# Optimization experiments

Hardware: AMD Instinct MI355X
Metric: run time of the kernel (lower is better)

## Reference

```python
import jax, jax.numpy as jnp
import numpy as np

D_MODEL = 2048
D_FF = 4096
N_EXPERTS = 8
TOP_K = 2
ALPHA = 0.01


def setup_inputs() -> dict:
    key = jax.random.key(0)
    ks = jax.random.split(key, 5)
    x = jax.random.normal(ks[0], (1, 2048, D_MODEL), dtype=jnp.float32)
    Wr = jax.random.normal(ks[1], (N_EXPERTS, D_MODEL), dtype=jnp.float32) * 0.01
    W1 = jax.random.normal(ks[2], (N_EXPERTS, D_MODEL, D_FF), dtype=jnp.float32) * (D_MODEL ** -0.5)
    W3 = jax.random.normal(ks[3], (N_EXPERTS, D_MODEL, D_FF), dtype=jnp.float32) * (D_MODEL ** -0.5)
    W2 = jax.random.normal(ks[4], (N_EXPERTS, D_FF, D_MODEL), dtype=jnp.float32) * (D_FF ** -0.5)
    return {"x": x, "Wr": Wr, "W1": W1, "W3": W3, "W2": W2}


def reference(x, Wr, W1, W3, W2):
    B, S, D = x.shape
    xf = x.reshape(-1, D)                      # [N, D]
    N = xf.shape[0]
    E = Wr.shape[0]
    logits = xf @ Wr.T                          # [N, E]
    probs = jax.nn.softmax(logits, axis=-1)
    tk_p, tk_i = jax.lax.top_k(probs, TOP_K)    # [N, K]
    tk_p = tk_p / tk_p.sum(axis=-1, keepdims=True)
    # combine weights per (token, expert); scatter-add matches masked sum over k
    w = jnp.zeros((N, E), x.dtype).at[jnp.arange(N)[:, None], tk_i].add(tk_p)
    # dense per-expert SwiGLU FFN (zero-weighted experts contribute nothing)
    gate = jnp.einsum('nd,edf->enf', xf, W1)    # [E, N, F]
    up = jnp.einsum('nd,edf->enf', xf, W3)
    expert_out = jnp.einsum('enf,efd->end', jax.nn.silu(gate) * up, W2)  # [E, N, D]
    out = jnp.einsum('ne,end->nd', w, expert_out).reshape(B, S, D)
    # load-balancing aux loss
    counts = jnp.zeros(E, x.dtype).at[tk_i.ravel()].add(1.0)
    f_i = counts / (N * TOP_K)
    P_i = probs.mean(axis=0)
    aux_loss = ALPHA * E * jnp.sum(f_i * P_i)
    return out, aux_loss
```

## Files before the change

kernel.cpp:

```cpp
#include <hip/hip_runtime.h>
#include <hip/hip_bf16.h>
#include <math.h>

#define D_MODEL 2048
#define D_FF    4096
#define NTOK    2048
#define NEXP    8
#define NPAIR   (NTOK*2)
#define MAXTILES 48

typedef __hip_bfloat16 bf16;
using frag_ab = __attribute__((ext_vector_type(8))) short;
using frag_cd = __attribute__((ext_vector_type(4))) float;

__device__ __forceinline__ short f2bf_s(float f) {
  __hip_bfloat16 h = __float2bfloat16(f);
  union { __hip_bfloat16 b; short s; } u; u.b = h; return u.s;
}
__device__ __forceinline__ short4 f2bf4(const float4 v) {
  short4 r; r.x = f2bf_s(v.x); r.y = f2bf_s(v.y); r.z = f2bf_s(v.z); r.w = f2bf_s(v.w);
  return r;
}
__device__ __forceinline__ frag_ab pack8(const float4 v0, const float4 v1) {
  frag_ab r;
  r[0] = f2bf_s(v0.x); r[1] = f2bf_s(v0.y); r[2] = f2bf_s(v0.z); r[3] = f2bf_s(v0.w);
  r[4] = f2bf_s(v1.x); r[5] = f2bf_s(v1.y); r[6] = f2bf_s(v1.z); r[7] = f2bf_s(v1.w);
  return r;
}
__device__ __forceinline__ void gload_lds16(const void* g, void* l) {
  __builtin_amdgcn_global_load_lds(
      (const __attribute__((address_space(1))) unsigned int*)g,
      (__attribute__((address_space(3))) unsigned int*)l, 16, 0, 0);
}

__global__ void k_zero(int* cnt, int* cur, float* psum) {
  int t = threadIdx.x;
  if (t < NEXP) { cnt[t] = 0; cur[t] = 0; psum[t] = 0.f; }
}

__global__ void k_route(const float* __restrict__ x, const float* __restrict__ Wr,
                        int* __restrict__ tki, float* __restrict__ tkw,
                        int* __restrict__ cnt, float* __restrict__ psum) {
  const int n = blockIdx.x;
  const int t = threadIdx.x;
  const float* xr = x + (size_t)n * D_MODEL;
  float acc[NEXP];
#pragma unroll
  for (int e = 0; e < NEXP; e++) acc[e] = 0.f;
  for (int d = t; d < D_MODEL; d += 256) {
    float xv = xr[d];
#pragma unroll
    for (int e = 0; e < NEXP; e++) acc[e] += xv * Wr[e * D_MODEL + d];
  }
  __shared__ float red[256 * NEXP];
#pragma unroll
  for (int e = 0; e < NEXP; e++) red[t * NEXP + e] = acc[e];
  __syncthreads();
  __shared__ float logit[NEXP];
  if (t < NEXP) {
    float s = 0.f;
    for (int i = 0; i < 256; i++) s += red[i * NEXP + t];
    logit[t] = s;
  }
  __syncthreads();
  if (t == 0) {
    float m = logit[0];
#pragma unroll
    for (int e = 1; e < NEXP; e++) m = fmaxf(m, logit[e]);
    float p[NEXP]; float s = 0.f;
#pragma unroll
    for (int e = 0; e < NEXP; e++) { p[e] = expf(logit[e] - m); s += p[e]; }
    float inv = 1.f / s;
#pragma unroll
    for (int e = 0; e < NEXP; e++) p[e] *= inv;
    int i0 = 0;
#pragma unroll
    for (int e = 1; e < NEXP; e++) if (p[e] > p[i0]) i0 = e;
    int i1 = (i0 == 0) ? 1 : 0;
#pragma unroll
    for (int e = 0; e < NEXP; e++) if (e != i0 && e != i1 && p[e] > p[i1]) i1 = e;
    float wsum = p[i0] + p[i1];
    tki[n*2]   = i0;          tki[n*2+1] = i1;
    tkw[n*2]   = p[i0]/wsum;  tkw[n*2+1] = p[i1]/wsum;
    atomicAdd(&cnt[i0], 1);   atomicAdd(&cnt[i1], 1);
#pragma unroll
    for (int e = 0; e < NEXP; e++) atomicAdd(&psum[e], p[e]);
  }
}

__global__ void k_scan(const int* __restrict__ cnt, const float* __restrict__ psum,
                       int* __restrict__ off, int* __restrict__ te, int* __restrict__ tm,
                       float* __restrict__ aux_out) {
  if (threadIdx.x != 0) return;
  int o = 0;
  for (int e = 0; e < NEXP; e++) { off[e] = o; o += cnt[e]; }
  off[NEXP] = o;
  int nt = 0;
  for (int e = 0; e < NEXP; e++)
    for (int msv = 0; msv < cnt[e]; msv += 128) { te[nt] = e; tm[nt] = msv; nt++; }
  for (; nt < MAXTILES; nt++) { te[nt] = -1; tm[nt] = 0; }
  float aux = 0.f;
  for (int e = 0; e < NEXP; e++)
    aux += ((float)cnt[e] / (float)NPAIR) * (psum[e] / (float)NTOK);
  aux_out[0] = aux * 0.01f * (float)NEXP;
}

__global__ void k_assign(const int* __restrict__ tki, const float* __restrict__ tkw,
                         const int* __restrict__ off, int* __restrict__ cur,
                         int* __restrict__ perm, float* __restrict__ pw,
                         int* __restrict__ posof) {
  int n = blockIdx.x * blockDim.x + threadIdx.x;
  if (n >= NTOK) return;
#pragma unroll
  for (int k = 0; k < 2; k++) {
    int e = tki[n*2+k];
    int r = atomicAdd(&cur[e], 1);
    int pos = off[e] + r;
    perm[pos] = n;
    pw[pos]   = tkw[n*2+k];
    posof[n*2+k] = pos;
  }
}

template<int K, int F>
__device__ __forceinline__ void tpose_body(const float* __restrict__ s,
                                           char* __restrict__ d,
                                           int k0, int f0, int t, float* T ) {
#pragma unroll
  for (int i = 0; i < 8; i++) {
    int sl = t + i * 256;
    int kr = sl >> 4, q4 = sl & 15;
    float4 v = *(const float4*)(s + (size_t)(k0 + kr) * F + f0 + q4 * 4);
    int qs = q4 ^ ((kr >> 3) & 7);
    *(float4*)(&T[kr * 64 + qs * 4]) = v;
  }
  __syncthreads();
#pragma unroll
  for (int i = 0; i < 4; i++) {
    int sl = t + i * 256;
    int fr = sl >> 4, cg = sl & 15;
    int g = cg >> 3, c = cg & 7;
    int l = c ^ (fr & 7);
    int rbase = g * 64 + l * 8;
    int col = (fr & 3) + (((fr >> 2) ^ l) << 2);
    frag_ab r;
#pragma unroll
    for (int j = 0; j < 8; j++) r[j] = f2bf_s(T[(rbase + j) * 64 + col]);
    *(frag_ab*)(d + (size_t)(f0 + fr) * K * 2 + (size_t)k0 * 2 + g * 128 + c * 16) = r;
  }
}

template<int K, int F>
__global__ __launch_bounds__(256) void k_tpose(const float* __restrict__ src,
                                               bf16* __restrict__ dst) {
  __shared__ __align__(16) float T[128 * 64];
  const int e = blockIdx.z;
  tpose_body<K, F>(src + (size_t)e * K * F, (char*)(dst + (size_t)e * F * K),
                   blockIdx.y * 128, blockIdx.x * 64, threadIdx.x, T);
}

template<int K, int F>
__global__ __launch_bounds__(256) void k_tpose_dual(const float* __restrict__ srcA,
                                                    const float* __restrict__ srcB,
                                                    bf16* __restrict__ dstA,
                                                    bf16* __restrict__ dstB) {
  __shared__ __align__(16) float T[128 * 64];
  const int e = blockIdx.z & 7;
  const float* src = (blockIdx.z & 8) ? srcB : srcA;
  bf16*        dst = (blockIdx.z & 8) ? dstB : dstA;
  tpose_body<K, F>(src + (size_t)e * K * F, (char*)(dst + (size_t)e * F * K),
                   blockIdx.y * 128, blockIdx.x * 64, threadIdx.x, T);
}

__global__ __launch_bounds__(256, 2) void k_gemm1n(
    const float* __restrict__ x, const bf16* __restrict__ W1b,
    const bf16* __restrict__ W3b,
    const int* __restrict__ perm, const int* __restrict__ off,
    const int* __restrict__ tile_e, const int* __restrict__ tile_m,
    const int* __restrict__ cnt, bf16* __restrict__ H) {
  const int e = tile_e[blockIdx.y];
  if (e < 0) return;
  const int ms = tile_m[blockIdx.y];
  int mrows = cnt[e] - ms; if (mrows > 128) mrows = 128;
  const int f0 = blockIdx.x * 128;
  const int base = off[e] + ms;

  __shared__ __align__(16) bf16 As [128 * 64];
  __shared__ __align__(16) bf16 B1s[128 * 64];
  __shared__ __align__(16) bf16 B3s[128 * 64];
  __shared__ int permS[128];

  const int t = threadIdx.x;
  const int lane = t & 63;
  const int wuni = t & 192;
  const int wid = t >> 6;
  const int wm = wid & 1, wn = wid >> 1;
  const int lm = lane & 15, q = lane >> 4;

  if (t < 128) permS[t] = (t < mrows) ? perm[base + t] : 0;

  frag_cd accg[4][4], accu[4][4];
#pragma unroll
  for (int i = 0; i < 4; i++)
#pragma unroll
    for (int j = 0; j < 4; j++) {
      accg[i][j] = {0.f,0.f,0.f,0.f};
      accu[i][j] = {0.f,0.f,0.f,0.f};
    }

  const char* W1e = (const char*)(W1b + (size_t)e * D_MODEL * D_FF);
  const char* W3e = (const char*)(W3b + (size_t)e * D_MODEL * D_FF);
  __syncthreads();

  for (int k0 = 0; k0 < D_MODEL; k0 += 64) {
#pragma unroll
    for (int i = 0; i < 4; i++) {
      int wslot = i * 256 + wuni;
      int slot  = wslot + lane;
      int row = slot >> 3, c = slot & 7;
      size_t gb = (size_t)(f0 + row) * (D_MODEL * 2) + (size_t)k0 * 2 + c * 16;
      gload_lds16(W1e + gb, &B1s[wslot * 8]);
      gload_lds16(W3e + gb, &B3s[wslot * 8]);
    }
#pragma unroll
    for (int i = 0; i < 4; i++) {
      int slot = i * 256 + t;
      int row = slot >> 3, c = slot & 7;
      int tok = permS[row];
      const float4* p = (const float4*)(x + (size_t)tok * D_MODEL + k0 + c * 8);
      frag_ab v = pack8(p[0], p[1]);
      *(frag_ab*)(&As[row * 64 + ((c ^ (row & 7)) * 8)]) = v;
    }
    __syncthreads();
#pragma unroll
    for (int ks = 0; ks < 2; ks++) {
      frag_ab a[4], b1[4], b3[4];
#pragma unroll
      for (int mf = 0; mf < 4; mf++) {
        int row = wm*64 + mf*16 + lm;
        int c = (ks*4 + q) ^ (row & 7);
        a[mf] = *(const frag_ab*)(&As[row * 64 + c * 8]);
      }
#pragma unroll
      for (int nf = 0; nf < 4; nf++) {
        int row = wn*64 + nf*16 + lm;
        int c = (ks*4 + q) ^ (row & 7);
        b1[nf] = *(const frag_ab*)(&B1s[row * 64 + c * 8]);
        b3[nf] = *(const frag_ab*)(&B3s[row * 64 + c * 8]);
      }
#pragma unroll
      for (int mf = 0; mf < 4; mf++)
#pragma unroll
        for (int nf = 0; nf < 4; nf++) {
          accg[mf][nf] = __builtin_amdgcn_mfma_f32_16x16x32_bf16(a[mf], b1[nf], accg[mf][nf], 0, 0, 0);
          accu[mf][nf] = __builtin_amdgcn_mfma_f32_16x16x32_bf16(a[mf], b3[nf], accu[mf][nf], 0, 0, 0);
        }
    }
    __syncthreads();
  }
#pragma unroll
  for (int mf = 0; mf < 4; mf++) {
#pragma unroll
    for (int r = 0; r < 4; r++) {
      int row = wm*64 + mf*16 + q*4 + r;
      if (row < mrows) {
        char* hrow = (char*)H + (size_t)(base + row) * (D_FF * 2);
        int key = row & 7;
#pragma unroll
        for (int nf = 0; nf < 4; nf++) {
          float g = accg[mf][nf][r];
          float u = accu[mf][nf][r];
          float h = g * u / (1.f + expf(-g));
          int f = f0 + wn*64 + nf*16 + lm;
          int grp = f >> 6, oct = (f >> 3) & 7, j = f & 7;
          *(bf16*)(hrow + grp*128 + ((oct ^ key) * 16) + j*2) = __float2bfloat16(h);
        }
      }
    }
  }
}

__global__ __launch_bounds__(256, 3) void k_gemm2n(
    const bf16* __restrict__ H, const bf16* __restrict__ W2b,
    const float* __restrict__ pw,
    const int* __restrict__ off, const int* __restrict__ tile_e,
    const int* __restrict__ tile_m, const int* __restrict__ cnt,
    float* __restrict__ eo) {
  const int e = tile_e[blockIdx.y];
  if (e < 0) return;
  const int ms = tile_m[blockIdx.y];
  int mrows = cnt[e] - ms; if (mrows > 128) mrows = 128;
  const int d0 = blockIdx.x * 128;
  const int base = off[e] + ms;

  __shared__ __align__(16) bf16 As[128 * 64];
  __shared__ __align__(16) bf16 Bs[128 * 64];

  const int t = threadIdx.x;
  const int lane = t & 63;
  const int wuni = t & 192;
  const int wid = t >> 6;
  const int wm = wid & 1, wn = wid >> 1;
  const int lm = lane & 15, q = lane >> 4;

  frag_cd acc[4][4];
#pragma unroll
  for (int i = 0; i < 4; i++)
#pragma unroll
    for (int j = 0; j < 4; j++) acc[i][j] = {0.f,0.f,0.f,0.f};

  const char* W2e = (const char*)(W2b + (size_t)e * D_FF * D_MODEL);
  const char* Hb  = (const char*)H;

  for (int k0 = 0; k0 < D_FF; k0 += 64) {
#pragma unroll
    for (int i = 0; i < 4; i++) {
      int wslot = i * 256 + wuni;
      int slot  = wslot + lane;
      int row = slot >> 3, c = slot & 7;
      gload_lds16(Hb + (size_t)(base + row) * (D_FF * 2) + (size_t)k0 * 2 + c * 16,
                  &As[wslot * 8]);
      gload_lds16(W2e + (size_t)(d0 + row) * (D_FF * 2) + (size_t)k0 * 2 + c * 16,
                  &Bs[wslot * 8]);
    }
    __syncthreads();
#pragma unroll
    for (int ks = 0; ks < 2; ks++) {
      frag_ab a[4], b[4];
#pragma unroll
      for (int mf = 0; mf < 4; mf++) {
        int row = wm*64 + mf*16 + lm;
        int c = (ks*4 + q) ^ (row & 7);
        a[mf] = *(const frag_ab*)(&As[row * 64 + c * 8]);
      }
#pragma unroll
      for (int nf = 0; nf < 4; nf++) {
        int row = wn*64 + nf*16 + lm;
        int c = (ks*4 + q) ^ (row & 7);
        b[nf] = *(const frag_ab*)(&Bs[row * 64 + c * 8]);
      }
#pragma unroll
      for (int mf = 0; mf < 4; mf++)
#pragma unroll
        for (int nf = 0; nf < 4; nf++)
          acc[mf][nf] = __builtin_amdgcn_mfma_f32_16x16x32_bf16(a[mf], b[nf], acc[mf][nf], 0, 0, 0);
    }
    __syncthreads();
  }
#pragma unroll
  for (int mf = 0; mf < 4; mf++) {
#pragma unroll
    for (int r = 0; r < 4; r++) {
      int row = wm*64 + mf*16 + q*4 + r;
      if (row < mrows) {
        float w = pw[base + row];
        float* orow = eo + (size_t)(base + row) * D_MODEL;
#pragma unroll
        for (int nf = 0; nf < 4; nf++)
          orow[d0 + wn*64 + nf*16 + lm] = w * acc[mf][nf][r];
      }
    }
  }
}

__global__ __launch_bounds__(256) void k_gemm1(
    const float* __restrict__ x, const float* __restrict__ W1,
    const float* __restrict__ W3,
    const int* __restrict__ perm, const int* __restrict__ off,
    const int* __restrict__ tile_e, const int* __restrict__ tile_m,
    const int* __restrict__ cnt, bf16* __restrict__ H) {
  const int e = tile_e[blockIdx.y];
  if (e < 0) return;
  const int ms = tile_m[blockIdx.y];
  int mrows = cnt[e] - ms; if (mrows > 128) mrows = 128;
  const int f0 = blockIdx.x * 128;
  const int base = off[e] + ms;

  __shared__ __align__(16) bf16 As [128 * 40];
  __shared__ __align__(16) bf16 B1s[128 * 40];
  __shared__ __align__(16) bf16 B3s[128 * 40];
  __shared__ int permS[128];

  const int t = threadIdx.x;
  const int lane = t & 63, wid = t >> 6;
  const int wm = wid & 1, wn = wid >> 1;
  const int lm = lane & 15, q = lane >> 4;

  if (t < 128) permS[t] = (t < mrows) ? perm[base + t] : 0;

  frag_cd accg[4][4], accu[4][4];
#pragma unroll
  for (int i = 0; i < 4; i++)
#pragma unroll
    for (int j = 0; j < 4; j++) {
      accg[i][j] = {0.f,0.f,0.f,0.f};
      accu[i][j] = {0.f,0.f,0.f,0.f};
    }

  const float* W1e = W1 + (size_t)e * D_MODEL * D_FF;
  const float* W3e = W3 + (size_t)e * D_MODEL * D_FF;
  __syncthreads();

  for (int k0 = 0; k0 < D_MODEL; k0 += 32) {
#pragma unroll
    for (int i = 0; i < 4; i++) {
      int s = t + i * 256;
      int row = s >> 3, kg = s & 7;
      float4 v = make_float4(0.f, 0.f, 0.f, 0.f);
      if (row < mrows) {
        int tok = permS[row];
        v = *(const float4*)(x + (size_t)tok * D_MODEL + k0 + kg * 4);
      }
      *(short4*)(&As[row * 40 + kg * 4]) = f2bf4(v);
    }
#pragma unroll
    for (int i = 0; i < 2; i++) {
      int s = t + i * 256;
      int f = s & 127, kg = s >> 7;
      const float* g1 = W1e + (size_t)(k0 + kg * 8) * D_FF + f0 + f;
      const float* g3 = W3e + (size_t)(k0 + kg * 8) * D_FF + f0 + f;
      short r1[8], r3[8];
#pragma unroll
      for (int j = 0; j < 8; j++) r1[j] = f2bf_s(g1[(size_t)j * D_FF]);
#pragma unroll
      for (int j = 0; j < 8; j++) r3[j] = f2bf_s(g3[(size_t)j * D_FF]);
      *(frag_ab*)(&B1s[f * 40 + kg * 8]) = *(const frag_ab*)r1;
      *(frag_ab*)(&B3s[f * 40 + kg * 8]) = *(const frag_ab*)r3;
    }
    __syncthreads();
    frag_ab a[4], b1[4], b3[4];
#pragma unroll
    for (int mf = 0; mf < 4; mf++)
      a[mf] = *(const frag_ab*)(&As[(wm*64 + mf*16 + lm) * 40 + q*8]);
#pragma unroll
    for (int nf = 0; nf < 4; nf++) {
      b1[nf] = *(const frag_ab*)(&B1s[(wn*64 + nf*16 + lm) * 40 + q*8]);
      b3[nf] = *(const frag_ab*)(&B3s[(wn*64 + nf*16 + lm) * 40 + q*8]);
    }
#pragma unroll
    for (int mf = 0; mf < 4; mf++)
#pragma unroll
      for (int nf = 0; nf < 4; nf++) {
        accg[mf][nf] = __builtin_amdgcn_mfma_f32_16x16x32_bf16(a[mf], b1[nf], accg[mf][nf], 0, 0, 0);
        accu[mf][nf] = __builtin_amdgcn_mfma_f32_16x16x32_bf16(a[mf], b3[nf], accu[mf][nf], 0, 0, 0);
      }
    __syncthreads();
  }
#pragma unroll
  for (int mf = 0; mf < 4; mf++) {
#pragma unroll
    for (int r = 0; r < 4; r++) {
      int row = wm*64 + mf*16 + q*4 + r;
      if (row < mrows) {
        bf16* hrow = H + (size_t)(base + row) * D_FF;
#pragma unroll
        for (int nf = 0; nf < 4; nf++) {
          float g = accg[mf][nf][r];
          float u = accu[mf][nf][r];
          float h = g * u / (1.f + expf(-g));
          hrow[f0 + wn*64 + nf*16 + lm] = __float2bfloat16(h);
        }
      }
    }
  }
}

__global__ __launch_bounds__(256) void k_gemm2(
    const bf16* __restrict__ H, const float* __restrict__ W2,
    const float* __restrict__ pw,
    const int* __restrict__ off, const int* __restrict__ tile_e,
    const int* __restrict__ tile_m, const int* __restrict__ cnt,
    float* __restrict__ eo) {
  const int e = tile_e[blockIdx.y];
  if (e < 0) return;
  const int ms = tile_m[blockIdx.y];
  int mrows = cnt[e] - ms; if (mrows > 128) mrows = 128;
  const int d0 = blockIdx.x * 128;
  const int base = off[e] + ms;

  __shared__ __align__(16) bf16 As[128 * 40];
  __shared__ __align__(16) bf16 Bs[128 * 40];

  const int t = threadIdx.x;
  const int lane = t & 63, wid = t >> 6;
  const int wm = wid & 1, wn = wid >> 1;
  const int lm = lane & 15, q = lane >> 4;

  frag_cd acc[4][4];
#pragma unroll
  for (int i = 0; i < 4; i++)
#pragma unroll
    for (int j = 0; j < 4; j++) acc[i][j] = {0.f,0.f,0.f,0.f};

  const float* W2e = W2 + (size_t)e * D_FF * D_MODEL;
  const short* Hs = (const short*)H;

  for (int k0 = 0; k0 < D_FF; k0 += 32) {
#pragma unroll
    for (int i = 0; i < 2; i++) {
      int s = t + i * 256;
      int row = s >> 2, kg = s & 3;
      frag_ab v = {0,0,0,0,0,0,0,0};
      if (row < mrows)
        v = *(const frag_ab*)(Hs + (size_t)(base + row) * D_FF + k0 + kg * 8);
      *(frag_ab*)(&As[row * 40 + kg * 8]) = v;
    }
#pragma unroll
    for (int i = 0; i < 2; i++) {
      int s = t + i * 256;
      int dd = s & 127, kg = s >> 7;
      const float* g2 = W2e + (size_t)(k0 + kg * 8) * D_MODEL + d0 + dd;
      short r2[8];
#pragma unroll
      for (int j = 0; j < 8; j++) r2[j] = f2bf_s(g2[(size_t)j * D_MODEL]);
      *(frag_ab*)(&Bs[dd * 40 + kg * 8]) = *(const frag_ab*)r2;
    }
    __syncthreads();
    frag_ab a[4], b[4];
#pragma unroll
    for (int mf = 0; mf < 4; mf++)
      a[mf] = *(const frag_ab*)(&As[(wm*64 + mf*16 + lm) * 40 + q*8]);
#pragma unroll
    for (int nf = 0; nf < 4; nf++)
      b[nf] = *(const frag_ab*)(&Bs[(wn*64 + nf*16 + lm) * 40 + q*8]);
#pragma unroll
    for (int mf = 0; mf < 4; mf++)
#pragma unroll
      for (int nf = 0; nf < 4; nf++)
        acc[mf][nf] = __builtin_amdgcn_mfma_f32_16x16x32_bf16(a[mf], b[nf], acc[mf][nf], 0, 0, 0);
    __syncthreads();
  }
#pragma unroll
  for (int mf = 0; mf < 4; mf++) {
#pragma unroll
    for (int r = 0; r < 4; r++) {
      int row = wm*64 + mf*16 + q*4 + r;
      if (row < mrows) {
        float w = pw[base + row];
        float* orow = eo + (size_t)(base + row) * D_MODEL;
#pragma unroll
        for (int nf = 0; nf < 4; nf++)
          orow[d0 + wn*64 + nf*16 + lm] = w * acc[mf][nf][r];
      }
    }
  }
}

__global__ void k_combine(const float* __restrict__ eo, const int* __restrict__ posof,
                          float* __restrict__ out) {
  int idx = blockIdx.x * 256 + threadIdx.x;
  int n = idx >> 9;
  int c = (idx & 511) * 4;
  int p0 = posof[n*2], p1 = posof[n*2+1];
  const float4 a = *(const float4*)(eo + (size_t)p0 * D_MODEL + c);
  const float4 b = *(const float4*)(eo + (size_t)p1 * D_MODEL + c);
  float4 r;
  r.x = a.x + b.x; r.y = a.y + b.y; r.z = a.z + b.z; r.w = a.w + b.w;
  *(float4*)(out + (size_t)n * D_MODEL + c) = r;
}

extern "C" void kernel_launch(void* const* d_in, const int* in_sizes, int n_in,
                              void* d_out, int out_size, void* d_ws, size_t ws_size,
                              hipStream_t stream) {
  const float* x  = (const float*)d_in[0];
  const float* Wr = (const float*)d_in[1];
  const float* W1 = (const float*)d_in[2];
  const float* W3 = (const float*)d_in[3];
  const float* W2 = (const float*)d_in[4];
  float* out = (float*)d_out;
  char* ws = (char*)d_ws;

  const size_t REQ = (290ull << 20);
  if (ws_size >= REQ) {
    bf16*  W1b = (bf16*)(ws);
    bf16*  W3b = (bf16*)(ws + (128ull << 20));
    bf16*  Hb  = (bf16*)(ws + (256ull << 20));
    bf16*  W2b = (bf16*)(ws);
    float* eo  = (float*)(ws + (128ull << 20));
    char*  ib  = ws + (289ull << 20);
    int*   perm  = (int*)(ib);
    float* pw    = (float*)(ib + 16384);
    int*   posof = (int*)(ib + 32768);
    int*   tki   = (int*)(ib + 49152);
    float* tkw   = (float*)(ib + 65536);
    int*   cnt   = (int*)(ib + 81920);
    int*   cur   = (int*)(ib + 82048);
    int*   off   = (int*)(ib + 82176);
    int*   te    = (int*)(ib + 82432);
    int*   tm    = (int*)(ib + 82688);
    float* psum  = (float*)(ib + 82944);

    k_zero<<<1, 64, 0, stream>>>(cnt, cur, psum);
    k_route<<<NTOK, 256, 0, stream>>>(x, Wr, tki, tkw, cnt, psum);
    k_scan<<<1, 1, 0, stream>>>(cnt, psum, off, te, tm, out + (size_t)NTOK * D_MODEL);
    k_assign<<<NTOK/256, 256, 0, stream>>>(tki, tkw, off, cur, perm, pw, posof);
    k_tpose_dual<D_MODEL, D_FF><<<dim3(D_FF/64, D_MODEL/128, 16), 256, 0, stream>>>(
        W1, W3, W1b, W3b);
    k_gemm1n<<<dim3(D_FF/128, MAXTILES), 256, 0, stream>>>(x, W1b, W3b, perm, off, te, tm, cnt, Hb);
    k_tpose<D_FF, D_MODEL><<<dim3(D_MODEL/64, D_FF/128, NEXP), 256, 0, stream>>>(W2, W2b);
    k_gemm2n<<<dim3(D_MODEL/128, MAXTILES), 256, 0, stream>>>(Hb, W2b, pw, off, te, tm, cnt, eo);
    k_combine<<<(NTOK*(D_MODEL/4))/256, 256, 0, stream>>>(eo, posof, out);
  } else {
    bf16*  H    = (bf16*)(ws);
    float* eo   = (float*)(ws + 33554432);
    char*  ib   = ws + 67108864;
    int*   perm  = (int*)(ib);
    float* pw    = (float*)(ib + 16384);
    int*   posof = (int*)(ib + 32768);
    int*   tki   = (int*)(ib + 49152);
    float* tkw   = (float*)(ib + 65536);
    int*   cnt   = (int*)(ib + 81920);
    int*   cur   = (int*)(ib + 82048);
    int*   off   = (int*)(ib + 82176);
    int*   te    = (int*)(ib + 82432);
    int*   tm    = (int*)(ib + 82688);
    float* psum  = (float*)(ib + 82944);

    k_zero<<<1, 64, 0, stream>>>(cnt, cur, psum);
    k_route<<<NTOK, 256, 0, stream>>>(x, Wr, tki, tkw, cnt, psum);
    k_scan<<<1, 1, 0, stream>>>(cnt, psum, off, te, tm, out + (size_t)NTOK * D_MODEL);
    k_assign<<<NTOK/256, 256, 0, stream>>>(tki, tkw, off, cur, perm, pw, posof);
    k_gemm1<<<dim3(D_FF/128, MAXTILES), 256, 0, stream>>>(x, W1, W3, perm, off, te, tm, cnt, H);
    k_gemm2<<<dim3(D_MODEL/128, MAXTILES), 256, 0, stream>>>(H, W2, pw, off, te, tm, cnt, eo);
    k_combine<<<(NTOK*(D_MODEL/4))/256, 256, 0, stream>>>(eo, posof, out);
  }
}
```

Before: 1.328 ms.

## Pre-convert activations to bf16 in router and stream them into GEMM1 via async LDS loads

The routing kernel now also writes a bf16 copy of x into workspace and uses a wavefront shuffle reduction instead of a 256-entry shared-memory reduction. A new GEMM1 variant gathers rows of this bf16 copy directly into LDS with global_load_lds, swizzled per row, replacing the per-tile fp32 load and conversion of x. This halves activation bytes read by GEMM1 and removes conversion work from its inner loop. In exchange it needs more workspace, adds a tier check, and keeps the old path when the workspace is too small.

```diff
diff --git a/kernel.cpp b/kernel.cpp
--- a/kernel.cpp
+++ b/kernel.cpp
@@ -40,10 +40,20 @@
 
 __global__ void k_route(const float* __restrict__ x, const float* __restrict__ Wr,
                         int* __restrict__ tki, float* __restrict__ tkw,
-                        int* __restrict__ cnt, float* __restrict__ psum) {
+                        int* __restrict__ cnt, float* __restrict__ psum,
+                        bf16* __restrict__ Xb) {
   const int n = blockIdx.x;
   const int t = threadIdx.x;
+  const int lane = t & 63, wid = t >> 6;
   const float* xr = x + (size_t)n * D_MODEL;
+  if (Xb) {
+    const float4* p4 = (const float4*)xr;
+    float4 v0 = p4[t];
+    float4 v1 = p4[t + 256];
+    char* xrow = (char*)Xb + (size_t)n * (D_MODEL * 2);
+    *(short4*)(xrow + t * 8)        = f2bf4(v0);
+    *(short4*)(xrow + 2048 + t * 8) = f2bf4(v1);
+  }
   float acc[NEXP];
 #pragma unroll
   for (int e = 0; e < NEXP; e++) acc[e] = 0.f;
@@ -52,16 +62,18 @@
 #pragma unroll
     for (int e = 0; e < NEXP; e++) acc[e] += xv * Wr[e * D_MODEL + d];
   }
-  __shared__ float red[256 * NEXP];
-#pragma unroll
-  for (int e = 0; e < NEXP; e++) red[t * NEXP + e] = acc[e];
+#pragma unroll
+  for (int e = 0; e < NEXP; e++)
+#pragma unroll
+    for (int off = 32; off > 0; off >>= 1)
+      acc[e] += __shfl_xor(acc[e], off, 64);
+  __shared__ float wred[4][NEXP];
+  if (lane == 0)
+#pragma unroll
+    for (int e = 0; e < NEXP; e++) wred[wid][e] = acc[e];
   __syncthreads();
   __shared__ float logit[NEXP];
-  if (t < NEXP) {
-    float s = 0.f;
-    for (int i = 0; i < 256; i++) s += red[i * NEXP + t];
-    logit[t] = s;
-  }
+  if (t < NEXP) logit[t] = wred[0][t] + wred[1][t] + wred[2][t] + wred[3][t];
   __syncthreads();
   if (t == 0) {
     float m = logit[0];
@@ -172,7 +184,117 @@
                    blockIdx.y * 128, blockIdx.x * 64, threadIdx.x, T);
 }
 
-__global__ __launch_bounds__(256, 2) void k_gemm1n(
+__global__ __launch_bounds__(256, 2) void k_gemm1x(
+    const bf16* __restrict__ Xb, const bf16* __restrict__ W1b,
+    const bf16* __restrict__ W3b,
+    const int* __restrict__ perm, const int* __restrict__ off,
+    const int* __restrict__ tile_e, const int* __restrict__ tile_m,
+    const int* __restrict__ cnt, bf16* __restrict__ H) {
+  const int e = tile_e[blockIdx.y];
+  if (e < 0) return;
+  const int ms = tile_m[blockIdx.y];
+  int mrows = cnt[e] - ms; if (mrows > 128) mrows = 128;
+  const int f0 = blockIdx.x * 128;
+  const int base = off[e] + ms;
+
+  __shared__ __align__(16) bf16 As [128 * 64];
+  __shared__ __align__(16) bf16 B1s[128 * 64];
+  __shared__ __align__(16) bf16 B3s[128 * 64];
+  __shared__ int permS[128];
+
+  const int t = threadIdx.x;
+  const int lane = t & 63;
+  const int wuni = t & 192;
+  const int wid = t >> 6;
+  const int wm = wid & 1, wn = wid >> 1;
+  const int lm = lane & 15, q = lane >> 4;
+
+  if (t < 128) permS[t] = (t < mrows) ? perm[base + t] : 0;
+
+  frag_cd accg[4][4], accu[4][4];
+#pragma unroll
+  for (int i = 0; i < 4; i++)
+#pragma unroll
+    for (int j = 0; j < 4; j++) {
+      accg[i][j] = {0.f,0.f,0.f,0.f};
+      accu[i][j] = {0.f,0.f,0.f,0.f};
+    }
+
+  const char* W1e = (const char*)(W1b + (size_t)e * D_MODEL * D_FF);
+  const char* W3e = (const char*)(W3b + (size_t)e * D_MODEL * D_FF);
+  const char* Xc  = (const char*)Xb;
+  __syncthreads();
+
+  size_t aoff[4];
+#pragma unroll
+  for (int i = 0; i < 4; i++) {
+    int slot = i * 256 + t;
+    int row = slot >> 3, c = slot & 7;
+    aoff[i] = (size_t)permS[row] * (D_MODEL * 2) + (size_t)((c ^ (row & 7)) * 16);
+  }
+
+  for (int k0 = 0; k0 < D_MODEL; k0 += 64) {
+    const size_t kb = (size_t)k0 * 2;
+#pragma unroll
+    for (int i = 0; i < 4; i++) {
+      int wslot = i * 256 + wuni;
+      int slot  = wslot + lane;
+      int row = slot >> 3, c = slot & 7;
+      size_t gb = (size_t)(f0 + row) * (D_MODEL * 2) + kb + c * 16;
+      gload_lds16(W1e + gb, &B1s[wslot * 8]);
+      gload_lds16(W3e + gb, &B3s[wslot * 8]);
+      gload_lds16(Xc + aoff[i] + kb, &As[wslot * 8]);
+    }
+    __syncthreads();
+#pragma unroll
+    for (int ks = 0; ks < 2; ks++) {
+      frag_ab a[4], b1[4], b3[4];
+#pragma unroll
+      for (int mf = 0; mf < 4; mf++) {
+        int row = wm*64 + mf*16 + lm;
+        int c = (ks*4 + q) ^ (row & 7);
+        a[mf] = *(const frag_ab*)(&As[row * 64 + c * 8]);
+      }
+#pragma unroll
+      for (int nf = 0; nf < 4; nf++) {
+        int row = wn*64 + nf*16 + lm;
+        int c = (ks*4 + q) ^ (row & 7);
+        b1[nf] = *(const frag_ab*)(&B1s[row * 64 + c * 8]);
+        b3[nf] = *(const frag_ab*)(&B3s[row * 64 + c * 8]);
+      }
+#pragma unroll
+      for (int mf = 0; mf < 4; mf++)
+#pragma unroll
+        for (int nf = 0; nf < 4; nf++) {
+          accg[mf][nf] = __builtin_amdgcn_mfma_f32_16x16x32_bf16(a[mf], b1[nf], accg[mf][nf], 0, 0, 0);
+          accu[mf][nf] = __builtin_amdgcn_mfma_f32_16x16x32_bf16(a[mf], b3[nf], accu[mf][nf], 0, 0, 0);
+        }
+    }
+    __syncthreads();
+  }
+#pragma unroll
+  for (int mf = 0; mf < 4; mf++) {
+#pragma unroll
+    for (int r = 0; r < 4; r++) {
+      int row = wm*64 + mf*16 + q*4 + r;
+      if (row < mrows) {
+        char* hrow = (char*)H + (size_t)(base + row) * (D_FF * 2);
+        int key = row & 7;
+#pragma unroll
+        for (int nf = 0; nf < 4; nf++) {
+          float g = accg[mf][nf][r];
+          float u = accu[mf][nf][r];
+          float h = g * u / (1.f + expf(-g));
+          int f = f0 + wn*64 + nf*16 + lm;
+          int grp = f >> 6, oct = (f >> 3) & 7, j = f & 7;
+          *(bf16*)(hrow + grp*128 + ((oct ^ key) * 16) + j*2) = __float2bfloat16(h);
+        }
+      }
+    }
+  }
+}
+
+__global__ __launch_bounds__(256, 2) void k_gemm1g(
     const float* __restrict__ x, const bf16* __restrict__ W1b,
     const bf16* __restrict__ W3b,
     const int* __restrict__ perm, const int* __restrict__ off,
@@ -570,14 +692,17 @@
   float* out = (float*)d_out;
   char* ws = (char*)d_ws;
 
-  const size_t REQ = (290ull << 20);
-  if (ws_size >= REQ) {
+  const size_t REQ1 = (304ull << 20);
+  const size_t REQ2 = (290ull << 20);
+  if (ws_size >= REQ2) {
+    const bool tier1 = (ws_size >= REQ1);
     bf16*  W1b = (bf16*)(ws);
     bf16*  W3b = (bf16*)(ws + (128ull << 20));
     bf16*  Hb  = (bf16*)(ws + (256ull << 20));
     bf16*  W2b = (bf16*)(ws);
     float* eo  = (float*)(ws + (128ull << 20));
-    char*  ib  = ws + (289ull << 20);
+    bf16*  Xb  = tier1 ? (bf16*)(ws + (288ull << 20)) : nullptr;
+    char*  ib  = ws + (tier1 ? (296ull << 20) : (289ull << 20));
     int*   perm  = (int*)(ib);
     float* pw    = (float*)(ib + 16384);
     int*   posof = (int*)(ib + 32768);
@@ -591,12 +716,15 @@
     float* psum  = (float*)(ib + 82944);
 
     k_zero<<<1, 64, 0, stream>>>(cnt, cur, psum);
-    k_route<<<NTOK, 256, 0, stream>>>(x, Wr, tki, tkw, cnt, psum);
+    k_route<<<NTOK, 256, 0, stream>>>(x, Wr, tki, tkw, cnt, psum, Xb);
     k_scan<<<1, 1, 0, stream>>>(cnt, psum, off, te, tm, out + (size_t)NTOK * D_MODEL);
     k_assign<<<NTOK/256, 256, 0, stream>>>(tki, tkw, off, cur, perm, pw, posof);
     k_tpose_dual<D_MODEL, D_FF><<<dim3(D_FF/64, D_MODEL/128, 16), 256, 0, stream>>>(
         W1, W3, W1b, W3b);
-    k_gemm1n<<<dim3(D_FF/128, MAXTILES), 256, 0, stream>>>(x, W1b, W3b, perm, off, te, tm, cnt, Hb);
+    if (tier1)
+      k_gemm1x<<<dim3(D_FF/128, MAXTILES), 256, 0, stream>>>(Xb, W1b, W3b, perm, off, te, tm, cnt, Hb);
+    else
+      k_gemm1g<<<dim3(D_FF/128, MAXTILES), 256, 0, stream>>>(x, W1b, W3b, perm, off, te, tm, cnt, Hb);
     k_tpose<D_FF, D_MODEL><<<dim3(D_MODEL/64, D_FF/128, NEXP), 256, 0, stream>>>(W2, W2b);
     k_gemm2n<<<dim3(D_MODEL/128, MAXTILES), 256, 0, stream>>>(Hb, W2b, pw, off, te, tm, cnt, eo);
     k_combine<<<(NTOK*(D_MODEL/4))/256, 256, 0, stream>>>(eo, posof, out);
@@ -617,7 +745,7 @@
     float* psum  = (float*)(ib + 82944);
 
     k_zero<<<1, 64, 0, stream>>>(cnt, cur, psum);
-    k_route<<<NTOK, 256, 0, stream>>>(x, Wr, tki, tkw, cnt, psum);
+    k_route<<<NTOK, 256, 0, stream>>>(x, Wr, tki, tkw, cnt, psum, nullptr);
     k_scan<<<1, 1, 0, stream>>>(cnt, psum, off, te, tm, out + (size_t)NTOK * D_MODEL);
     k_assign<<<NTOK/256, 256, 0, stream>>>(tki, tkw, off, cur, perm, pw, posof);
     k_gemm1<<<dim3(D_FF/128, MAXTILES), 256, 0, stream>>>(x, W1, W3, perm, off, te, tm, cnt, H);
```

Measured after the change: 1.297 ms. 2.3% less time.
